# Optimization experiments

Measured on AMD Instinct MI355X. Metric: run time of the kernel, lower is better.

## Reference

```python
import jax, jax.numpy as jnp
import numpy as np

N_HEAD = 16
QMIN, QMAX = 0.0, 255.0  # 8-bit asymmetric


def fake_quantize(x, scale, zp):
    # LearnableFakeQuantize (asymmetric, 8-bit) with straight-through round.
    q = x / scale + zp
    q = q + jax.lax.stop_gradient(jnp.round(q) - q)  # STE round
    q = jnp.clip(q, QMIN, QMAX)
    return (q - zp) * scale


def setup_inputs() -> dict:
    key = jax.random.key(0)
    ks = jax.random.split(key, 4)
    B, T, C = 2, 2048, 1024
    return {
        "hidden_states": jax.random.normal(ks[0], (B, T, C), jnp.float32),
        "W_attn": jax.random.normal(ks[1], (C, 3 * C), jnp.float32) * (1.0 / np.sqrt(C)),
        "b_attn": jnp.zeros((3 * C,), jnp.float32),
        "W_proj": jax.random.normal(ks[2], (C, C), jnp.float32) * (1.0 / np.sqrt(C)),
        "b_proj": jnp.zeros((C,), jnp.float32),
        "kv_scale": jnp.full((1,), 0.05, jnp.float32),
        "kv_zp": jnp.full((1,), 128.0, jnp.float32),
    }


def reference(hidden_states, W_attn, b_attn, W_proj, b_proj, kv_scale, kv_zp):
    B, T, C = hidden_states.shape
    H = N_HEAD
    D = C // H
    qkv = hidden_states @ W_attn + b_attn            # [B,T,3C]
    q, k, v = jnp.split(qkv, 3, axis=2)
    # [B,T,C] -> [B,H,T,D]
    q = q.reshape(B, T, H, D).transpose(0, 2, 1, 3)
    k = k.reshape(B, T, H, D).transpose(0, 2, 1, 3)
    v = v.reshape(B, T, H, D).transpose(0, 2, 1, 3)
    k = fake_quantize(k, kv_scale, kv_zp)
    v = fake_quantize(v, kv_scale, kv_zp)
    scores = jnp.einsum("bhqd,bhkd->bhqk", q, k) / jnp.sqrt(jnp.asarray(D, q.dtype))
    causal = jnp.tril(jnp.ones((T, T), bool))        # bias[:T,:T]
    scores = jnp.where(causal, scores, jnp.asarray(-jnp.inf, scores.dtype))
    attn = jax.nn.softmax(scores, axis=-1)
    out = jnp.einsum("bhqk,bhkd->bhqd", attn, v)     # [B,H,T,D]
    out = out.transpose(0, 2, 1, 3).reshape(B, T, C)
    return out @ W_proj + b_proj
```

## Files before the change

### kernel.cpp

```cpp
#include <hip/hip_runtime.h>
#include <math.h>

#define TB 2048
#define CC 1024
#define NH 16
#define HD 64

typedef __bf16 bf16x8 __attribute__((ext_vector_type(8)));
typedef __bf16 bf16x4 __attribute__((ext_vector_type(4)));
typedef float  f32x4  __attribute__((ext_vector_type(4)));

__device__ inline float exp2fast(float x) { return __builtin_amdgcn_exp2f(x); }

__device__ __forceinline__ void gl_lds16(const __bf16* g, __bf16* l) {
    __builtin_amdgcn_global_load_lds(
        (const __attribute__((address_space(1))) void*)g,
        (__attribute__((address_space(3))) void*)l, 16, 0, 0);
}

__global__ __launch_bounds__(256)
void prep_kernel(const float* __restrict__ hidden, __bf16* __restrict__ hb,
                 const float* __restrict__ Wa, __bf16* __restrict__ wat,
                 const float* __restrict__ Wp, __bf16* __restrict__ wpt)
{
    __shared__ __bf16 L[64][68];
    const int tid = threadIdx.x;
    const int bid = blockIdx.x;
    if (bid < 4096) {
        int i = (bid * 256 + tid) * 4;
        f32x4 v = *(const f32x4*)&hidden[i];
        bf16x4 o;
        o.x = (__bf16)v.x; o.y = (__bf16)v.y; o.z = (__bf16)v.z; o.w = (__bf16)v.w;
        *(bf16x4*)&hb[i] = o;
        return;
    }
    const float* src; __bf16* dst; int N, n0, k0;
    if (bid < 4096 + 768) {
        int t = bid - 4096;
        src = Wa; dst = wat; N = 3072;
        n0 = (t % 48) * 64; k0 = (t / 48) * 64;
    } else {
        int t = bid - 4864;
        src = Wp; dst = wpt; N = 1024;
        n0 = (t % 16) * 64; k0 = (t / 16) * 64;
    }
    #pragma unroll
    for (int i = 0; i < 4; i++) {
        int id = tid + i * 256;
        int r = id >> 4, c = (id & 15) * 4;
        f32x4 v = *(const f32x4*)&src[(size_t)(k0 + r) * N + n0 + c];
        bf16x4 o;
        o.x = (__bf16)v.x; o.y = (__bf16)v.y; o.z = (__bf16)v.z; o.w = (__bf16)v.w;
        *(bf16x4*)&L[r][c] = o;
    }
    __syncthreads();
    #pragma unroll
    for (int i = 0; i < 4; i++) {
        int id = tid + i * 256;
        int nr = id >> 4, kc = (id & 15) * 4;
        bf16x4 o;
        o.x = L[kc + 0][nr]; o.y = L[kc + 1][nr];
        o.z = L[kc + 2][nr]; o.w = L[kc + 3][nr];
        *(bf16x4*)&dst[(size_t)(n0 + nr) * 1024 + k0 + kc] = o;
    }
}

template<int BN, int MODE>
__global__ __launch_bounds__(256)
void gemm_bt(const __bf16* __restrict__ A, const __bf16* __restrict__ Bt,
             const float* __restrict__ bias,
             __bf16* __restrict__ o0, __bf16* __restrict__ o1,
             __bf16* __restrict__ o2, float* __restrict__ of,
             int M, int N, int K,
             const float* __restrict__ scp, const float* __restrict__ zpp)
{
    constexpr int NT = BN / 32;
    __shared__ __bf16 Asm[128][64];
    __shared__ __bf16 Bsm[BN][64];

    const int tid  = threadIdx.x;
    const int m0   = blockIdx.y * 128;
    const int n0   = blockIdx.x * BN;
    const int w    = tid >> 6, lane = tid & 63;
    const int wm   = (w & 1) * 64, wn = (w >> 1) * (BN / 2);
    const int r16  = lane & 15, quad = lane >> 4;
    const int srow = lane >> 3;
    const int scol = ((lane & 7) ^ srow) * 8;
    const int rsw  = r16 & 7;

    f32x4 acc[NT][4];
    #pragma unroll
    for (int i = 0; i < NT; i++)
        #pragma unroll
        for (int j = 0; j < 4; j++) acc[i][j] = 0.f;

    for (int k0 = 0; k0 < K; k0 += 64) {
        #pragma unroll
        for (int p = 0; p < 4; p++)
            gl_lds16(&A[(size_t)(m0 + w * 32 + p * 8 + srow) * K + k0 + scol],
                     &Asm[w * 32 + p * 8][0]);
        #pragma unroll
        for (int p = 0; p < BN / 32; p++)
            gl_lds16(&Bt[(size_t)(n0 + w * (BN / 4) + p * 8 + srow) * K + k0 + scol],
                     &Bsm[w * (BN / 4) + p * 8][0]);
        __syncthreads();

        #pragma unroll
        for (int ks = 0; ks < 2; ks++) {
            const int col = ((ks * 4 + quad) ^ rsw) * 8;
            bf16x8 af[4], bfr[NT];
            #pragma unroll
            for (int mt = 0; mt < 4; mt++)
                af[mt] = *(const bf16x8*)&Asm[wm + mt * 16 + r16][col];
            #pragma unroll
            for (int nt = 0; nt < NT; nt++)
                bfr[nt] = *(const bf16x8*)&Bsm[wn + nt * 16 + r16][col];
            #pragma unroll
            for (int nt = 0; nt < NT; nt++)
                #pragma unroll
                for (int mt = 0; mt < 4; mt++)
                    acc[nt][mt] = __builtin_amdgcn_mfma_f32_16x16x32_bf16(
                        bfr[nt], af[mt], acc[nt][mt], 0, 0, 0);
        }
        __syncthreads();
    }

    const float sc = scp[0];
    const float zp = zpp[0];

    #pragma unroll
    for (int nt = 0; nt < NT; nt++) {
        #pragma unroll
        for (int mt = 0; mt < 4; mt++) {
            int gm = m0 + wm + mt * 16 + r16;
            int gn = n0 + wn + nt * 16 + quad * 4;
            f32x4 val = acc[nt][mt] + *(const f32x4*)&bias[gn];
            if (MODE == 1) {
                *(f32x4*)&of[(size_t)gm * N + gn] = val;
            } else {
                int part = gn >> 10;
                int idx  = gn & 1023;
                int h = idx >> 6, d = idx & 63;
                int b = gm >> 11, t = gm & 2047;
                size_t off = (((size_t)(b * NH + h)) * TB + t) * HD + d;
                bf16x4 st;
                if (part == 0) {
                    #pragma unroll
                    for (int r = 0; r < 4; r++)
                        st[r] = (__bf16)(val[r] * 0.18033688f);
                    *(bf16x4*)&o0[off] = st;
                } else {
                    #pragma unroll
                    for (int r = 0; r < 4; r++) {
                        float qv = val[r] / sc + zp;
                        qv = rintf(qv);
                        qv = fminf(fmaxf(qv, 0.f), 255.f);
                        st[r] = (__bf16)((qv - zp) * sc);
                    }
                    if (part == 1) *(bf16x4*)&o1[off] = st;
                    else           *(bf16x4*)&o2[off] = st;
                }
            }
        }
    }
}

__global__ __launch_bounds__(512, 4)
void attn_mfma(const __bf16* __restrict__ Q, const __bf16* __restrict__ Kg,
               const __bf16* __restrict__ Vg, __bf16* __restrict__ O)
{
    __shared__ alignas(16) __bf16 Ksm[64][72];
    __shared__ alignas(16) __bf16 Vsm[64][72];

    const int tid  = threadIdx.x;
    const int p    = blockIdx.x >> 5;
    const int bh   = blockIdx.x & 31;
    const int w    = tid >> 6, lane = tid & 63;
    const int wq   = w & 3;
    const int qt   = (w < 4) ? (31 - p) : p;
    const int ktmax = 31 - p;
    const int q0   = qt * 64;
    const int l15  = lane & 15, quad = lane >> 4;
    const int b    = bh >> 4, h = bh & 15;

    const int krow = tid >> 3;
    const int kseg = (tid & 7) * 8;
    const int vkey = tid & 63;
    const int vc   = tid >> 6;

    const __bf16* Kbh = Kg + (size_t)bh * TB * HD;
    const __bf16* Vbh = Vg + (size_t)bh * TB * HD;

    const __bf16* Qrow = Q + ((size_t)bh * TB + q0 + wq * 16 + l15) * HD;
    bf16x8 qf0 = *(const bf16x8*)&Qrow[quad * 8];
    bf16x8 qf1 = *(const bf16x8*)&Qrow[32 + quad * 8];

    const int rbase = (l15 >> 2) * 8 + (l15 & 3);

    bf16x8 af_l;
    {
        __bf16 v = (l15 == 0) ? (__bf16)1.0f : (__bf16)0.0f;
        #pragma unroll
        for (int j = 0; j < 8; j++) af_l[j] = v;
    }

    f32x4 acc_o[4], acc_l;
    #pragma unroll
    for (int nt = 0; nt < 4; nt++) acc_o[nt] = 0.f;
    acc_l = 0.f;
    float mrun = -3.0e38f;

    bf16x8 kpre = *(const bf16x8*)&Kbh[(size_t)krow * HD + kseg];
    bf16x8 vpre = *(const bf16x8*)&Vbh[(size_t)vkey * HD + vc * 8];

    for (int kt = 0; kt <= ktmax; kt++) {
        __syncthreads();
        *(bf16x8*)&Ksm[krow][kseg] = kpre;
        #pragma unroll
        for (int j = 0; j < 8; j++)
            Vsm[vc * 8 + j][vkey] = vpre[j];
        __syncthreads();

        if (kt < ktmax) {
            const __bf16* Kn = Kbh + (size_t)(kt + 1) * 64 * HD;
            const __bf16* Vn = Vbh + (size_t)(kt + 1) * 64 * HD;
            kpre = *(const bf16x8*)&Kn[(size_t)krow * HD + kseg];
            vpre = *(const bf16x8*)&Vn[(size_t)vkey * HD + vc * 8];
        }

        if (kt > qt) continue;

        const bool diag = (kt == qt);

        f32x4 s[4];
        #pragma unroll
        for (int nt = 0; nt < 4; nt++) s[nt] = 0.f;
        __builtin_amdgcn_s_setprio(1);
        #pragma unroll
        for (int nt = 0; nt < 4; nt++) {
            if (diag && (nt & 1) && wq < 2) continue;
            int row = rbase + (nt & 1) * 32 + ((nt >> 1) << 2);
            bf16x8 kf0 = *(const bf16x8*)&Ksm[row][quad * 8];
            bf16x8 kf1 = *(const bf16x8*)&Ksm[row][32 + quad * 8];
            s[nt] = __builtin_amdgcn_mfma_f32_16x16x32_bf16(kf0, qf0, s[nt], 0, 0, 0);
            s[nt] = __builtin_amdgcn_mfma_f32_16x16x32_bf16(kf1, qf1, s[nt], 0, 0, 0);
        }
        __builtin_amdgcn_s_setprio(0);

        if (diag) {
            #pragma unroll
            for (int nt = 0; nt < 4; nt++) {
                int koff = (nt & 1) * 32 + ((nt >> 1) << 2) + quad * 8;
                #pragma unroll
                for (int r = 0; r < 4; r++)
                    if (koff + r > wq * 16 + l15) s[nt][r] = -3.0e38f;
            }
        }

        float m0 = fmaxf(fmaxf(s[0][0], s[0][1]), fmaxf(s[0][2], s[0][3]));
        float m1 = fmaxf(fmaxf(s[1][0], s[1][1]), fmaxf(s[1][2], s[1][3]));
        float m2 = fmaxf(fmaxf(s[2][0], s[2][1]), fmaxf(s[2][2], s[2][3]));
        float m3 = fmaxf(fmaxf(s[3][0], s[3][1]), fmaxf(s[3][2], s[3][3]));
        float mx = fmaxf(fmaxf(m0, m1), fmaxf(m2, m3));
        mx = fmaxf(mx, __shfl_xor(mx, 16));
        mx = fmaxf(mx, __shfl_xor(mx, 32));

        float mnew  = fmaxf(mrun, mx);
        float alpha = exp2fast(mrun - mnew);
        mrun = mnew;
        #pragma unroll
        for (int nt = 0; nt < 4; nt++)
            #pragma unroll
            for (int r = 0; r < 4; r++) acc_o[nt][r] *= alpha;
        acc_l[0] *= alpha;

        float pv[4][4];
        #pragma unroll
        for (int nt = 0; nt < 4; nt++)
            #pragma unroll
            for (int r = 0; r < 4; r++) pv[nt][r] = exp2fast(s[nt][r] - mnew);

        bf16x8 pf0, pf1;
        #pragma unroll
        for (int j = 0; j < 4; j++) {
            pf0[j]     = (__bf16)pv[0][j];
            pf0[4 + j] = (__bf16)pv[2][j];
            pf1[j]     = (__bf16)pv[1][j];
            pf1[4 + j] = (__bf16)pv[3][j];
        }

        __builtin_amdgcn_s_setprio(1);
        acc_l = __builtin_amdgcn_mfma_f32_16x16x32_bf16(af_l, pf0, acc_l, 0, 0, 0);
        acc_l = __builtin_amdgcn_mfma_f32_16x16x32_bf16(af_l, pf1, acc_l, 0, 0, 0);

        #pragma unroll
        for (int nt = 0; nt < 4; nt++) {
            bf16x8 vf0 = *(const bf16x8*)&Vsm[nt * 16 + l15][quad * 8];
            bf16x8 vf1 = *(const bf16x8*)&Vsm[nt * 16 + l15][32 + quad * 8];
            acc_o[nt] = __builtin_amdgcn_mfma_f32_16x16x32_bf16(vf0, pf0, acc_o[nt], 0, 0, 0);
            acc_o[nt] = __builtin_amdgcn_mfma_f32_16x16x32_bf16(vf1, pf1, acc_o[nt], 0, 0, 0);
        }
        __builtin_amdgcn_s_setprio(0);
    }

    float lall = __shfl(acc_l[0], l15);
    float inv  = 1.f / lall;
    size_t trow = (size_t)(b * TB) + q0 + wq * 16 + l15;
    #pragma unroll
    for (int nt = 0; nt < 4; nt++) {
        bf16x4 st;
        #pragma unroll
        for (int r = 0; r < 4; r++) st[r] = (__bf16)(acc_o[nt][r] * inv);
        *(bf16x4*)&O[trow * CC + h * HD + nt * 16 + quad * 4] = st;
    }
}

extern "C" void kernel_launch(void* const* d_in, const int* in_sizes, int n_in,
                              void* d_out, int out_size, void* d_ws, size_t ws_size,
                              hipStream_t stream) {
    (void)in_sizes; (void)n_in; (void)out_size; (void)ws_size;
    const float* hidden   = (const float*)d_in[0];
    const float* W_attn   = (const float*)d_in[1];
    const float* b_attn   = (const float*)d_in[2];
    const float* W_proj   = (const float*)d_in[3];
    const float* b_proj   = (const float*)d_in[4];
    const float* kv_scale = (const float*)d_in[5];
    const float* kv_zp    = (const float*)d_in[6];
    float* out = (float*)d_out;

    __bf16* hb  = (__bf16*)d_ws;
    __bf16* wat = hb  + (size_t)4096 * 1024;
    __bf16* wpt = wat + (size_t)3072 * 1024;
    __bf16* qws = wpt + (size_t)1024 * 1024;
    __bf16* kws = qws + (size_t)2 * NH * TB * HD;
    __bf16* vws = kws + (size_t)2 * NH * TB * HD;
    __bf16* ows = vws + (size_t)2 * NH * TB * HD;

    prep_kernel<<<5120, 256, 0, stream>>>(hidden, hb, W_attn, wat, W_proj, wpt);

    gemm_bt<128, 0><<<dim3(24, 32), 256, 0, stream>>>(
        hb, wat, b_attn, qws, kws, vws, nullptr, 4096, 3072, 1024, kv_scale, kv_zp);

    attn_mfma<<<dim3(16 * 32), 512, 0, stream>>>(qws, kws, vws, ows);

    gemm_bt<64, 1><<<dim3(16, 32), 256, 0, stream>>>(
        ows, wpt, b_proj, nullptr, nullptr, nullptr, out, 4096, 1024, 1024,
        kv_scale, kv_zp);
}
```

Baseline: 180.6 us.

## Double-buffer K/V shared memory tiles to drop one barrier per iteration

The K/V tiles in shared memory become two buffers. The next tile is stored into the alternate buffer while the current one is consumed, and global prefetch runs two tiles ahead. This removes one __syncthreads per key-tile iteration and overlaps the LDS stores with compute. The row padding also changes from 72 to 76, which alters the bank-conflict pattern and may misalign the 16-byte vector loads. LDS use doubles, which could lower occupancy at 4 blocks per CU.

```diff
diff --git a/kernel.cpp b/kernel.cpp
--- a/kernel.cpp
+++ b/kernel.cpp
@@ -169,8 +169,8 @@
 void attn_mfma(const __bf16* __restrict__ Q, const __bf16* __restrict__ Kg,
                const __bf16* __restrict__ Vg, __bf16* __restrict__ O)
 {
-    __shared__ alignas(16) __bf16 Ksm[64][72];
-    __shared__ alignas(16) __bf16 Vsm[64][72];
+    __shared__ alignas(16) __bf16 Ksm[2][64][76];
+    __shared__ alignas(16) __bf16 Vsm[2][64][76];
 
     const int tid  = threadIdx.x;
     const int p    = blockIdx.x >> 5;
@@ -212,95 +212,109 @@
 
     bf16x8 kpre = *(const bf16x8*)&Kbh[(size_t)krow * HD + kseg];
     bf16x8 vpre = *(const bf16x8*)&Vbh[(size_t)vkey * HD + vc * 8];
+    *(bf16x8*)&Ksm[0][krow][kseg] = kpre;
+    #pragma unroll
+    for (int j = 0; j < 8; j++)
+        Vsm[0][vc * 8 + j][vkey] = vpre[j];
+    {
+        const __bf16* Kn = Kbh + (size_t)64 * HD;
+        const __bf16* Vn = Vbh + (size_t)64 * HD;
+        kpre = *(const bf16x8*)&Kn[(size_t)krow * HD + kseg];
+        vpre = *(const bf16x8*)&Vn[(size_t)vkey * HD + vc * 8];
+    }
+    __syncthreads();
 
     for (int kt = 0; kt <= ktmax; kt++) {
+        const int cur = kt & 1;
+
+        if (kt < ktmax) {
+            *(bf16x8*)&Ksm[cur ^ 1][krow][kseg] = kpre;
+            #pragma unroll
+            for (int j = 0; j < 8; j++)
+                Vsm[cur ^ 1][vc * 8 + j][vkey] = vpre[j];
+            if (kt + 1 < ktmax) {
+                const __bf16* Kn = Kbh + (size_t)(kt + 2) * 64 * HD;
+                const __bf16* Vn = Vbh + (size_t)(kt + 2) * 64 * HD;
+                kpre = *(const bf16x8*)&Kn[(size_t)krow * HD + kseg];
+                vpre = *(const bf16x8*)&Vn[(size_t)vkey * HD + vc * 8];
+            }
+        }
+
+        if (kt <= qt) {
+            const bool diag = (kt == qt);
+
+            f32x4 s[4];
+            #pragma unroll
+            for (int nt = 0; nt < 4; nt++) s[nt] = 0.f;
+            __builtin_amdgcn_s_setprio(1);
+            #pragma unroll
+            for (int nt = 0; nt < 4; nt++) {
+                if (diag && (nt & 1) && wq < 2) continue;
+                int row = rbase + (nt & 1) * 32 + ((nt >> 1) << 2);
+                bf16x8 kf0 = *(const bf16x8*)&Ksm[cur][row][quad * 8];
+                bf16x8 kf1 = *(const bf16x8*)&Ksm[cur][row][32 + quad * 8];
+                s[nt] = __builtin_amdgcn_mfma_f32_16x16x32_bf16(kf0, qf0, s[nt], 0, 0, 0);
+                s[nt] = __builtin_amdgcn_mfma_f32_16x16x32_bf16(kf1, qf1, s[nt], 0, 0, 0);
+            }
+            __builtin_amdgcn_s_setprio(0);
+
+            if (diag) {
+                #pragma unroll
+                for (int nt = 0; nt < 4; nt++) {
+                    int koff = (nt & 1) * 32 + ((nt >> 1) << 2) + quad * 8;
+                    #pragma unroll
+                    for (int r = 0; r < 4; r++)
+                        if (koff + r > wq * 16 + l15) s[nt][r] = -3.0e38f;
+                }
+            }
+
+            float m0 = fmaxf(fmaxf(s[0][0], s[0][1]), fmaxf(s[0][2], s[0][3]));
+            float m1 = fmaxf(fmaxf(s[1][0], s[1][1]), fmaxf(s[1][2], s[1][3]));
+            float m2 = fmaxf(fmaxf(s[2][0], s[2][1]), fmaxf(s[2][2], s[2][3]));
+            float m3 = fmaxf(fmaxf(s[3][0], s[3][1]), fmaxf(s[3][2], s[3][3]));
+            float mx = fmaxf(fmaxf(m0, m1), fmaxf(m2, m3));
+            mx = fmaxf(mx, __shfl_xor(mx, 16));
+            mx = fmaxf(mx, __shfl_xor(mx, 32));
+
+            float mnew  = fmaxf(mrun, mx);
+            float alpha = exp2fast(mrun - mnew);
+            mrun = mnew;
+            #pragma unroll
+            for (int nt = 0; nt < 4; nt++)
+                #pragma unroll
+                for (int r = 0; r < 4; r++) acc_o[nt][r] *= alpha;
+            acc_l[0] *= alpha;
+
+            float pv[4][4];
+            #pragma unroll
+            for (int nt = 0; nt < 4; nt++)
+                #pragma unroll
+                for (int r = 0; r < 4; r++) pv[nt][r] = exp2fast(s[nt][r] - mnew);
+
+            bf16x8 pf0, pf1;
+            #pragma unroll
+            for (int j = 0; j < 4; j++) {
+                pf0[j]     = (__bf16)pv[0][j];
+                pf0[4 + j] = (__bf16)pv[2][j];
+                pf1[j]     = (__bf16)pv[1][j];
+                pf1[4 + j] = (__bf16)pv[3][j];
+            }
+
+            __builtin_amdgcn_s_setprio(1);
+            acc_l = __builtin_amdgcn_mfma_f32_16x16x32_bf16(af_l, pf0, acc_l, 0, 0, 0);
+            acc_l = __builtin_amdgcn_mfma_f32_16x16x32_bf16(af_l, pf1, acc_l, 0, 0, 0);
+
+            #pragma unroll
+            for (int nt = 0; nt < 4; nt++) {
+                bf16x8 vf0 = *(const bf16x8*)&Vsm[cur][nt * 16 + l15][quad * 8];
+                bf16x8 vf1 = *(const bf16x8*)&Vsm[cur][nt * 16 + l15][32 + quad * 8];
+                acc_o[nt] = __builtin_amdgcn_mfma_f32_16x16x32_bf16(vf0, pf0, acc_o[nt], 0, 0, 0);
+                acc_o[nt] = __builtin_amdgcn_mfma_f32_16x16x32_bf16(vf1, pf1, acc_o[nt], 0, 0, 0);
+            }
+            __builtin_amdgcn_s_setprio(0);
+        }
+
         __syncthreads();
-        *(bf16x8*)&Ksm[krow][kseg] = kpre;
-        #pragma unroll
-        for (int j = 0; j < 8; j++)
-            Vsm[vc * 8 + j][vkey] = vpre[j];
-        __syncthreads();
-
-        if (kt < ktmax) {
-            const __bf16* Kn = Kbh + (size_t)(kt + 1) * 64 * HD;
-            const __bf16* Vn = Vbh + (size_t)(kt + 1) * 64 * HD;
-            kpre = *(const bf16x8*)&Kn[(size_t)krow * HD + kseg];
-            vpre = *(const bf16x8*)&Vn[(size_t)vkey * HD + vc * 8];
-        }
-
-        if (kt > qt) continue;
-
-        const bool diag = (kt == qt);
-
-        f32x4 s[4];
-        #pragma unroll
-        for (int nt = 0; nt < 4; nt++) s[nt] = 0.f;
-        __builtin_amdgcn_s_setprio(1);
-        #pragma unroll
-        for (int nt = 0; nt < 4; nt++) {
-            if (diag && (nt & 1) && wq < 2) continue;
-            int row = rbase + (nt & 1) * 32 + ((nt >> 1) << 2);
-            bf16x8 kf0 = *(const bf16x8*)&Ksm[row][quad * 8];
-            bf16x8 kf1 = *(const bf16x8*)&Ksm[row][32 + quad * 8];
-            s[nt] = __builtin_amdgcn_mfma_f32_16x16x32_bf16(kf0, qf0, s[nt], 0, 0, 0);
-            s[nt] = __builtin_amdgcn_mfma_f32_16x16x32_bf16(kf1, qf1, s[nt], 0, 0, 0);
-        }
-        __builtin_amdgcn_s_setprio(0);
-
-        if (diag) {
-            #pragma unroll
-            for (int nt = 0; nt < 4; nt++) {
-                int koff = (nt & 1) * 32 + ((nt >> 1) << 2) + quad * 8;
-                #pragma unroll
-                for (int r = 0; r < 4; r++)
-                    if (koff + r > wq * 16 + l15) s[nt][r] = -3.0e38f;
-            }
-        }
-
-        float m0 = fmaxf(fmaxf(s[0][0], s[0][1]), fmaxf(s[0][2], s[0][3]));
-        float m1 = fmaxf(fmaxf(s[1][0], s[1][1]), fmaxf(s[1][2], s[1][3]));
-        float m2 = fmaxf(fmaxf(s[2][0], s[2][1]), fmaxf(s[2][2], s[2][3]));
-        float m3 = fmaxf(fmaxf(s[3][0], s[3][1]), fmaxf(s[3][2], s[3][3]));
-        float mx = fmaxf(fmaxf(m0, m1), fmaxf(m2, m3));
-        mx = fmaxf(mx, __shfl_xor(mx, 16));
-        mx = fmaxf(mx, __shfl_xor(mx, 32));
-
-        float mnew  = fmaxf(mrun, mx);
-        float alpha = exp2fast(mrun - mnew);
-        mrun = mnew;
-        #pragma unroll
-        for (int nt = 0; nt < 4; nt++)
-            #pragma unroll
-            for (int r = 0; r < 4; r++) acc_o[nt][r] *= alpha;
-        acc_l[0] *= alpha;
-
-        float pv[4][4];
-        #pragma unroll
-        for (int nt = 0; nt < 4; nt++)
-            #pragma unroll
-            for (int r = 0; r < 4; r++) pv[nt][r] = exp2fast(s[nt][r] - mnew);
-
-        bf16x8 pf0, pf1;
-        #pragma unroll
-        for (int j = 0; j < 4; j++) {
-            pf0[j]     = (__bf16)pv[0][j];
-            pf0[4 + j] = (__bf16)pv[2][j];
-            pf1[j]     = (__bf16)pv[1][j];
-            pf1[4 + j] = (__bf16)pv[3][j];
-        }
-
-        __builtin_amdgcn_s_setprio(1);
-        acc_l = __builtin_amdgcn_mfma_f32_16x16x32_bf16(af_l, pf0, acc_l, 0, 0, 0);
-        acc_l = __builtin_amdgcn_mfma_f32_16x16x32_bf16(af_l, pf1, acc_l, 0, 0, 0);
-
-        #pragma unroll
-        for (int nt = 0; nt < 4; nt++) {
-            bf16x8 vf0 = *(const bf16x8*)&Vsm[nt * 16 + l15][quad * 8];
-            bf16x8 vf1 = *(const bf16x8*)&Vsm[nt * 16 + l15][32 + quad * 8];
-            acc_o[nt] = __builtin_amdgcn_mfma_f32_16x16x32_bf16(vf0, pf0, acc_o[nt], 0, 0, 0);
-            acc_o[nt] = __builtin_amdgcn_mfma_f32_16x16x32_bf16(vf1, pf1, acc_o[nt], 0, 0, 0);
-        }
-        __builtin_amdgcn_s_setprio(0);
     }
 
     float lall = __shfl(acc_l[0], l15);
```

Result: slower. 185.4 us (+2.7%).
